# Kernel optimization log

Measured on AMD Instinct MI355X. Metric: run time of the kernel, lower is better.

The kernel has to match this reference:

```python
import jax, jax.numpy as jnp
import numpy as np

N, D, K = 131072, 128, 256
MAX_ITER = 8
TOL = 1e-4


def setup_inputs() -> dict:
    key = jax.random.key(0)
    kx, kp = jax.random.split(key)
    X = jax.random.normal(kx, (N, D), dtype=jnp.float32)
    # torch.randperm(N)[:K] -> distinct initial centroid indices
    init_idx = jax.random.permutation(kp, N)[:K]
    return {"X": X, "init_idx": init_idx, "max_iter": MAX_ITER}


def _assign(X, centroids):
    # argmin over Euclidean distance == argmin over squared distance;
    # ||x||^2 is constant per row so drop it: d2[n,k] = ||c_k||^2 - 2 x_n . c_k
    d2 = jnp.sum(centroids * centroids, axis=1)[None, :] - 2.0 * (X @ centroids.T)  # [N,K]
    return jnp.argmin(d2, axis=1)  # [N]


def reference(X, init_idx, max_iter):
    n = X.shape[0]
    centroids0 = X[init_idx]  # [K,D]

    def step(carry, _):
        centroids, done = carry
        labels = _assign(X, centroids)  # [N]
        sums = jax.ops.segment_sum(X, labels, num_segments=K)  # [K,D]
        counts = jax.ops.segment_sum(jnp.ones((n,), X.dtype), labels, num_segments=K)  # [K]
        new_c = sums / counts[:, None]  # empty cluster -> 0/0 = nan (matches torch mean of empty)
        shift = jnp.linalg.norm(new_c - centroids)
        new_done = jnp.logical_or(done, shift < TOL)
        # torch breaks BEFORE assigning new centroids when converged
        centroids = jnp.where(new_done, centroids, new_c)
        return (centroids, new_done), labels

    (centroids, _), labels_hist = jax.lax.scan(
        step, (centroids0, jnp.array(False)), None, length=max_iter
    )
    labels = labels_hist[-1]
    return labels, centroids
```

## Files before the change

kernel.cpp:

```cpp
#include <hip/hip_runtime.h>

#define NP 131072
#define DD 128
#define KK 256
#define MAXIT 8
#define TOLSQ (1e-4f * 1e-4f)
#define POSB 256
#define UPIPE 8

typedef _Float16 half8 __attribute__((ext_vector_type(8)));
typedef float f32x4 __attribute__((ext_vector_type(4)));

__device__ __forceinline__ void async_copy16(const void* g, void* l) {
    __builtin_amdgcn_global_load_lds(
        (const __attribute__((address_space(1))) void*)g,
        (__attribute__((address_space(3))) void*)l, 16, 0, 0);
}

struct Ws {
    float C[KK * DD];
    float newC[KK * DD];
    float cnorm[KK];
    float sums[KK * DD];
    float shiftsq;
    int done;
    int ilab[NP];
    int counts[KK];
    int cursor[KK];
    int ordlab[NP];
    alignas(16) _Float16 Csh[KK * DD];
    alignas(16) _Float16 Csl[KK * DD];
    alignas(16) _Float16 Xsh[(size_t)NP * DD];
    alignas(16) _Float16 Xsl[(size_t)NP * DD];
};

__global__ void k_init(const float* __restrict__ X, const int* __restrict__ idx,
                       float* __restrict__ C, int* __restrict__ done) {
    int k = blockIdx.x, d = threadIdx.x;
    C[k * DD + d] = X[(size_t)idx[k] * DD + d];
    if (k == 0 && d == 0) *done = 0;
}

__global__ void k_split(const float* __restrict__ X, _Float16* __restrict__ Xh,
                        _Float16* __restrict__ Xl) {
    size_t idx = (size_t)blockIdx.x * 256 + threadIdx.x;
    int lane = idx & 63;
    size_t g16k = idx >> 6;
    size_t point = (g16k >> 2) * 16 + (lane & 15);
    int dim0 = (int)(g16k & 3) * 32 + (lane >> 4) * 8;
    const f32x4* s4 = (const f32x4*)(X + point * DD + dim0);
    f32x4 a = s4[0], b = s4[1];
    half8 h, l;
#pragma unroll
    for (int j = 0; j < 4; j++) {
        _Float16 hi = (_Float16)a[j];
        h[j] = hi; l[j] = (_Float16)(a[j] - (float)hi);
    }
#pragma unroll
    for (int j = 0; j < 4; j++) {
        _Float16 hi = (_Float16)b[j];
        h[4 + j] = hi; l[4 + j] = (_Float16)(b[j] - (float)hi);
    }
    *(half8*)(Xh + idx * 8) = h;
    *(half8*)(Xl + idx * 8) = l;
}

__global__ void k_prep0(const float* __restrict__ C, float* __restrict__ cnorm,
                        _Float16* __restrict__ Ch, _Float16* __restrict__ Cl,
                        int* __restrict__ counts, int* __restrict__ cursor) {
    int k = blockIdx.x, d = threadIdx.x;
    float v = C[k * DD + d];
    _Float16 hi = (_Float16)v;
    int ct = k >> 4, l4 = k & 15, ks = d >> 5, q = (d >> 3) & 3, j = d & 7;
    size_t dst = ((size_t)(ks * 16 + ct) * 64 + (q * 16 + l4)) * 8 + j;
    Ch[dst] = hi;
    Cl[dst] = (_Float16)(v - (float)hi);
    __shared__ float red[DD];
    red[d] = v * v;
    __syncthreads();
    for (int s = DD / 2; s > 0; s >>= 1) {
        if (d < s) red[d] += red[d + s];
        __syncthreads();
    }
    if (d == 0) {
        cnorm[k] = red[0];
        counts[k] = 0;
        cursor[k] = 0;
    }
}

__global__ __launch_bounds__(256, 2) void k_assign(
    const _Float16* __restrict__ Xh, const _Float16* __restrict__ Xl,
    const _Float16* __restrict__ Ch, const _Float16* __restrict__ Cl,
    const float* __restrict__ cnorm, float* __restrict__ outlab,
    int* __restrict__ ilab, int* __restrict__ counts,
    float* __restrict__ shiftsq) {
    __shared__ __align__(16) _Float16 Bls[2 * 2 * 16 * 64 * 8];
    __shared__ int hist[KK];
    if (blockIdx.x == 0 && threadIdx.x == 0) *shiftsq = 0.0f;
    hist[threadIdx.x] = 0;

    const int wave = threadIdx.x >> 6;
    const int lane = threadIdx.x & 63;
    const int l4 = lane & 15, g = lane >> 4;
    const int g16 = blockIdx.x * 8 + wave * 2;
    char* const lds = (char*)Bls;

    auto stage = [&](int ks, int buf) {
        char* dst = lds + buf * 32768;
#pragma unroll
        for (int j = 0; j < 4; j++) {
            const int slot = j * 256 + wave * 64;
            async_copy16(Ch + (size_t)ks * 8192 + (size_t)(slot + lane) * 8,
                         dst + (size_t)slot * 16);
            async_copy16(Cl + (size_t)ks * 8192 + (size_t)(slot + lane) * 8,
                         dst + 16384 + (size_t)slot * 16);
        }
    };

    f32x4 acc[2][16];
#pragma unroll
    for (int pg = 0; pg < 2; pg++)
#pragma unroll
        for (int ct = 0; ct < 16; ct++) acc[pg][ct] = (f32x4){0.f, 0.f, 0.f, 0.f};

    stage(0, 0);
    __syncthreads();

#pragma unroll 1
    for (int ks = 0; ks < 4; ks++) {
        if (ks < 3) stage(ks + 1, (ks + 1) & 1);

        const size_t a0 = ((size_t)(g16 * 4 + ks) * 64 + lane) * 8;
        const size_t a1 = ((size_t)((g16 + 1) * 4 + ks) * 64 + lane) * 8;
        half8 ah0 = *(const half8*)(Xh + a0);
        half8 al0 = *(const half8*)(Xl + a0);
        half8 ah1 = *(const half8*)(Xh + a1);
        half8 al1 = *(const half8*)(Xl + a1);

        char* cur = lds + (ks & 1) * 32768;
#pragma unroll
        for (int ct = 0; ct < 16; ct++) {
            half8 bh = *(const half8*)(cur + ct * 1024 + lane * 16);
            half8 bl = *(const half8*)(cur + 16384 + ct * 1024 + lane * 16);
            acc[0][ct] = __builtin_amdgcn_mfma_f32_16x16x32_f16(al0, bh, acc[0][ct], 0, 0, 0);
            acc[0][ct] = __builtin_amdgcn_mfma_f32_16x16x32_f16(ah0, bl, acc[0][ct], 0, 0, 0);
            acc[0][ct] = __builtin_amdgcn_mfma_f32_16x16x32_f16(ah0, bh, acc[0][ct], 0, 0, 0);
            acc[1][ct] = __builtin_amdgcn_mfma_f32_16x16x32_f16(al1, bh, acc[1][ct], 0, 0, 0);
            acc[1][ct] = __builtin_amdgcn_mfma_f32_16x16x32_f16(ah1, bl, acc[1][ct], 0, 0, 0);
            acc[1][ct] = __builtin_amdgcn_mfma_f32_16x16x32_f16(ah1, bh, acc[1][ct], 0, 0, 0);
        }
        __syncthreads();
    }

    float cn[16];
#pragma unroll
    for (int ct = 0; ct < 16; ct++) cn[ct] = cnorm[ct * 16 + l4];

    unsigned long long best[2][4];
#pragma unroll
    for (int pg = 0; pg < 2; pg++)
#pragma unroll
        for (int r = 0; r < 4; r++) best[pg][r] = ~0ull;

#pragma unroll
    for (int pg = 0; pg < 2; pg++)
#pragma unroll
        for (int ct = 0; ct < 16; ct++)
#pragma unroll
            for (int r = 0; r < 4; r++) {
                float s = fmaf(-2.0f, acc[pg][ct][r], cn[ct]);
                if (__builtin_isnan(s)) s = -__builtin_inff();
                unsigned u = __float_as_uint(s);
                unsigned m = (u >> 31) ? ~u : (u ^ 0x80000000u);
                unsigned long long key =
                    ((unsigned long long)m << 32) | (unsigned)(ct * 16 + l4);
                if (key < best[pg][r]) best[pg][r] = key;
            }

#pragma unroll
    for (int d = 1; d < 16; d <<= 1)
#pragma unroll
        for (int pg = 0; pg < 2; pg++)
#pragma unroll
            for (int r = 0; r < 4; r++) {
                unsigned long long o = __shfl_xor(best[pg][r], d, 64);
                if (o < best[pg][r]) best[pg][r] = o;
            }

    __syncthreads();
    if (l4 == 0) {
#pragma unroll
        for (int pg = 0; pg < 2; pg++)
#pragma unroll
            for (int r = 0; r < 4; r++) {
                int point = blockIdx.x * 128 + wave * 32 + pg * 16 + g * 4 + r;
                int lbl = (int)(best[pg][r] & 0x1ff);
                outlab[point] = (float)lbl;
                ilab[point] = lbl;
                atomicAdd(&hist[lbl], 1);
            }
    }
    __syncthreads();
    int h = hist[threadIdx.x];
    if (h) atomicAdd(&counts[threadIdx.x], h);
}

__global__ __launch_bounds__(256) void k_scatter(
    const int* __restrict__ ilab, const int* __restrict__ counts,
    int* __restrict__ cursor, int* __restrict__ ordlab,
    float* __restrict__ sums) {
    const int t = threadIdx.x;
    const int b = blockIdx.x;

    if (t < 128) sums[b * 128 + t] = 0.0f;

    __shared__ int hist[KK];
    __shared__ int pre[KK];
    __shared__ int gbase[KK];
    hist[t] = 0;
    int c = counts[t];
    pre[t] = c;
    __syncthreads();

    const int p0 = b * 512;
    const int la = ilab[p0 + t];
    const int lb = ilab[p0 + 256 + t];
    atomicAdd(&hist[la], 1);
    atomicAdd(&hist[lb], 1);

#pragma unroll
    for (int d = 1; d < KK; d <<= 1) {
        int v = (t >= d) ? pre[t - d] : 0;
        __syncthreads();
        pre[t] += v;
        __syncthreads();
    }
    int h = hist[t];
    int gb = (pre[t] - c) + (h ? atomicAdd(&cursor[t], h) : 0);
    gbase[t] = gb;
    __syncthreads();
    hist[t] = 0;
    __syncthreads();

    int ra = atomicAdd(&hist[la], 1);
    ordlab[gbase[la] + ra] = (p0 + t) | (la << 17);
    int rb = atomicAdd(&hist[lb], 1);
    ordlab[gbase[lb] + rb] = (p0 + 256 + t) | (lb << 17);
}

__global__ __launch_bounds__(256) void k_sum(
    const float* __restrict__ X, const int* __restrict__ ordlab,
    float* __restrict__ sums) {
    const int t = threadIdx.x;
    const int d = t & 127, h = t >> 7;

    __shared__ int sol[POSB];
    sol[t] = ordlab[blockIdx.x * POSB + t];
    __syncthreads();

    const int PP = POSB / 2;
    float xv[UPIPE], xn[UPIPE];
#pragma unroll
    for (int u = 0; u < UPIPE; u++)
        xv[u] = X[(size_t)(sol[2 * u + h] & 0x1ffff) * DD + d];

    float acc = 0.0f;
    int cur = sol[h] >> 17;

    for (int jb = 0; jb < PP; jb += UPIPE) {
#pragma unroll
        for (int u = 0; u < UPIPE; u++) {
            int nj = jb + u + UPIPE;
            int o = sol[2 * (nj < PP ? nj : PP - 1) + h];
            xn[u] = X[(size_t)(o & 0x1ffff) * DD + d];
        }
#pragma unroll
        for (int u = 0; u < UPIPE; u++) {
            int l = sol[2 * (jb + u) + h] >> 17;
            if (l != cur) {
                atomicAdd(&sums[cur * DD + d], acc);
                acc = 0.0f;
                cur = l;
            }
            acc += xv[u];
        }
#pragma unroll
        for (int u = 0; u < UPIPE; u++) xv[u] = xn[u];
    }
    atomicAdd(&sums[cur * DD + d], acc);
}

__global__ void k_reduce(const float* __restrict__ sums, const int* __restrict__ counts,
                         const float* __restrict__ C, float* __restrict__ newC,
                         float* __restrict__ shiftsq) {
    const int g = blockIdx.x * 256 + threadIdx.x;
    const int k = g >> 7;
    const int t = threadIdx.x;

    float nc = sums[g] / (float)counts[k];
    newC[g] = nc;
    float diff = nc - C[g];

    __shared__ float red[256];
    red[t] = diff * diff;
    __syncthreads();
    for (int st = 128; st > 0; st >>= 1) {
        if (t < st) red[t] += red[t + st];
        __syncthreads();
    }
    if (t == 0) atomicAdd(shiftsq, red[0]);
}

__global__ void k_upprep(const float* __restrict__ newC, float* __restrict__ C,
                         const float* __restrict__ shiftsq, int* __restrict__ done,
                         float* __restrict__ cnorm, _Float16* __restrict__ Ch,
                         _Float16* __restrict__ Cl, int* __restrict__ counts,
                         int* __restrict__ cursor) {
    const int t = threadIdx.x;
    const int k = blockIdx.x * 2 + (t >> 7);
    const int d = t & 127;
    float ss = *shiftsq;
    int nd = (*done != 0) || (ss < TOLSQ);
    float v = nd ? C[k * DD + d] : newC[k * DD + d];
    C[k * DD + d] = v;
    if (blockIdx.x == 0 && t == 0 && nd) *done = 1;
    if (d == 0) {
        counts[k] = 0;
        cursor[k] = 0;
    }

    _Float16 hi = (_Float16)v;
    int ct = k >> 4, l4 = k & 15, ks = d >> 5, q = (d >> 3) & 3, j = d & 7;
    size_t dst = ((size_t)(ks * 16 + ct) * 64 + (q * 16 + l4)) * 8 + j;
    Ch[dst] = hi;
    Cl[dst] = (_Float16)(v - (float)hi);

    __shared__ float red[256];
    red[t] = v * v;
    __syncthreads();
    for (int s = 64; s > 0; s >>= 1) {
        if ((t & 127) < s) red[t] += red[t + s];
        __syncthreads();
    }
    if (d == 0) cnorm[k] = red[t];
}

__global__ void k_final(const float* __restrict__ C, float* __restrict__ out) {
    int i = blockIdx.x * 256 + threadIdx.x;
    out[i] = C[i];
}

extern "C" void kernel_launch(void* const* d_in, const int* in_sizes, int n_in,
                              void* d_out, int out_size, void* d_ws, size_t ws_size,
                              hipStream_t stream) {
    const float* X = (const float*)d_in[0];
    const int* idx = (const int*)d_in[1];
    float* out = (float*)d_out;
    Ws* w = (Ws*)d_ws;

    k_init<<<KK, DD, 0, stream>>>(X, idx, w->C, &w->done);
    k_split<<<(int)((size_t)NP * DD / 8 / 256), 256, 0, stream>>>(X, w->Xsh, w->Xsl);
    k_prep0<<<KK, DD, 0, stream>>>(w->C, w->cnorm, w->Csh, w->Csl, w->counts, w->cursor);

    for (int it = 0; it < MAXIT; it++) {
        k_assign<<<NP / 128, 256, 0, stream>>>(w->Xsh, w->Xsl, w->Csh, w->Csl,
                                               w->cnorm, out, w->ilab, w->counts,
                                               &w->shiftsq);
        k_scatter<<<NP / 512, 256, 0, stream>>>(w->ilab, w->counts, w->cursor,
                                                w->ordlab, w->sums);
        k_sum<<<NP / POSB, 256, 0, stream>>>(X, w->ordlab, w->sums);
        k_reduce<<<KK * DD / 256, 256, 0, stream>>>(w->sums, w->counts, w->C,
                                                    w->newC, &w->shiftsq);
        k_upprep<<<KK / 2, 256, 0, stream>>>(w->newC, w->C, &w->shiftsq, &w->done,
                                             w->cnorm, w->Csh, w->Csl, w->counts,
                                             w->cursor);
    }

    k_final<<<KK * DD / 256, 256, 0, stream>>>(w->C, out + NP);
}
```

Measured before the change: 723.5 us.

## Load all centroids into LDS once per block and loop over point tiles

The assign kernel now runs 512-thread blocks that copy the full split-fp16 centroid matrix (128 KB) into LDS once, then each wave processes two point tiles. This replaces per-k-slice double-buffered staging and the syncthreads between slices, and register-prefetches the next X slice. It amortises centroid loads over four times more points per block and removes barriers. The cost is a 128 KB LDS footprint, which may limit occupancy to one block per CU despite the launch bounds requesting two.

```diff
diff --git a/kernel.cpp b/kernel.cpp
--- a/kernel.cpp
+++ b/kernel.cpp
@@ -89,121 +89,132 @@
     }
 }
 
-__global__ __launch_bounds__(256, 2) void k_assign(
+__global__ __launch_bounds__(512, 2) void k_assign(
     const _Float16* __restrict__ Xh, const _Float16* __restrict__ Xl,
     const _Float16* __restrict__ Ch, const _Float16* __restrict__ Cl,
     const float* __restrict__ cnorm, float* __restrict__ outlab,
     int* __restrict__ ilab, int* __restrict__ counts,
     float* __restrict__ shiftsq) {
-    __shared__ __align__(16) _Float16 Bls[2 * 2 * 16 * 64 * 8];
+    __shared__ __align__(16) _Float16 B[2 * KK * DD];
     __shared__ int hist[KK];
-    if (blockIdx.x == 0 && threadIdx.x == 0) *shiftsq = 0.0f;
-    hist[threadIdx.x] = 0;
-
-    const int wave = threadIdx.x >> 6;
-    const int lane = threadIdx.x & 63;
+    const int tid = threadIdx.x;
+    const int wave = tid >> 6;
+    const int lane = tid & 63;
     const int l4 = lane & 15, g = lane >> 4;
-    const int g16 = blockIdx.x * 8 + wave * 2;
-    char* const lds = (char*)Bls;
-
-    auto stage = [&](int ks, int buf) {
-        char* dst = lds + buf * 32768;
-#pragma unroll
-        for (int j = 0; j < 4; j++) {
-            const int slot = j * 256 + wave * 64;
-            async_copy16(Ch + (size_t)ks * 8192 + (size_t)(slot + lane) * 8,
-                         dst + (size_t)slot * 16);
-            async_copy16(Cl + (size_t)ks * 8192 + (size_t)(slot + lane) * 8,
-                         dst + 16384 + (size_t)slot * 16);
-        }
-    };
-
-    f32x4 acc[2][16];
-#pragma unroll
-    for (int pg = 0; pg < 2; pg++)
-#pragma unroll
-        for (int ct = 0; ct < 16; ct++) acc[pg][ct] = (f32x4){0.f, 0.f, 0.f, 0.f};
-
-    stage(0, 0);
+
+    if (blockIdx.x == 0 && tid == 0) *shiftsq = 0.0f;
+    if (tid < KK) hist[tid] = 0;
+
+    char* const lds = (char*)B;
+#pragma unroll
+    for (int r = 0; r < 8; r++) {
+        const int slot = r * 512 + wave * 64;
+        async_copy16(Ch + (size_t)(slot + lane) * 8, lds + (size_t)slot * 16);
+        async_copy16(Cl + (size_t)(slot + lane) * 8,
+                     lds + 65536 + (size_t)slot * 16);
+    }
+
+    float cn[16];
+#pragma unroll
+    for (int ct = 0; ct < 16; ct++) cn[ct] = cnorm[ct * 16 + l4];
+
     __syncthreads();
 
 #pragma unroll 1
-    for (int ks = 0; ks < 4; ks++) {
-        if (ks < 3) stage(ks + 1, (ks + 1) & 1);
-
-        const size_t a0 = ((size_t)(g16 * 4 + ks) * 64 + lane) * 8;
-        const size_t a1 = ((size_t)((g16 + 1) * 4 + ks) * 64 + lane) * 8;
+    for (int t = 0; t < 2; t++) {
+        const int g16 = blockIdx.x * 32 + t * 16 + wave * 2;
+
+        f32x4 acc[2][16];
+#pragma unroll
+        for (int pg = 0; pg < 2; pg++)
+#pragma unroll
+            for (int ct = 0; ct < 16; ct++) acc[pg][ct] = (f32x4){0.f, 0.f, 0.f, 0.f};
+
+        size_t a0 = ((size_t)(g16 * 4 + 0) * 64 + lane) * 8;
+        size_t a1 = ((size_t)((g16 + 1) * 4 + 0) * 64 + lane) * 8;
         half8 ah0 = *(const half8*)(Xh + a0);
         half8 al0 = *(const half8*)(Xl + a0);
         half8 ah1 = *(const half8*)(Xh + a1);
         half8 al1 = *(const half8*)(Xl + a1);
 
-        char* cur = lds + (ks & 1) * 32768;
-#pragma unroll
-        for (int ct = 0; ct < 16; ct++) {
-            half8 bh = *(const half8*)(cur + ct * 1024 + lane * 16);
-            half8 bl = *(const half8*)(cur + 16384 + ct * 1024 + lane * 16);
-            acc[0][ct] = __builtin_amdgcn_mfma_f32_16x16x32_f16(al0, bh, acc[0][ct], 0, 0, 0);
-            acc[0][ct] = __builtin_amdgcn_mfma_f32_16x16x32_f16(ah0, bl, acc[0][ct], 0, 0, 0);
-            acc[0][ct] = __builtin_amdgcn_mfma_f32_16x16x32_f16(ah0, bh, acc[0][ct], 0, 0, 0);
-            acc[1][ct] = __builtin_amdgcn_mfma_f32_16x16x32_f16(al1, bh, acc[1][ct], 0, 0, 0);
-            acc[1][ct] = __builtin_amdgcn_mfma_f32_16x16x32_f16(ah1, bl, acc[1][ct], 0, 0, 0);
-            acc[1][ct] = __builtin_amdgcn_mfma_f32_16x16x32_f16(ah1, bh, acc[1][ct], 0, 0, 0);
+#pragma unroll 1
+        for (int ks = 0; ks < 4; ks++) {
+            half8 nh0, nl0, nh1, nl1;
+            if (ks < 3) {
+                const size_t b0 = ((size_t)(g16 * 4 + ks + 1) * 64 + lane) * 8;
+                const size_t b1 = ((size_t)((g16 + 1) * 4 + ks + 1) * 64 + lane) * 8;
+                nh0 = *(const half8*)(Xh + b0);
+                nl0 = *(const half8*)(Xl + b0);
+                nh1 = *(const half8*)(Xh + b1);
+                nl1 = *(const half8*)(Xl + b1);
+            }
+
+            char* const curh = lds + ks * 16384;
+            char* const curl = lds + 65536 + ks * 16384;
+#pragma unroll
+            for (int ct = 0; ct < 16; ct++) {
+                half8 bh = *(const half8*)(curh + ct * 1024 + lane * 16);
+                half8 bl = *(const half8*)(curl + ct * 1024 + lane * 16);
+                acc[0][ct] = __builtin_amdgcn_mfma_f32_16x16x32_f16(al0, bh, acc[0][ct], 0, 0, 0);
+                acc[0][ct] = __builtin_amdgcn_mfma_f32_16x16x32_f16(ah0, bl, acc[0][ct], 0, 0, 0);
+                acc[0][ct] = __builtin_amdgcn_mfma_f32_16x16x32_f16(ah0, bh, acc[0][ct], 0, 0, 0);
+                acc[1][ct] = __builtin_amdgcn_mfma_f32_16x16x32_f16(al1, bh, acc[1][ct], 0, 0, 0);
+                acc[1][ct] = __builtin_amdgcn_mfma_f32_16x16x32_f16(ah1, bl, acc[1][ct], 0, 0, 0);
+                acc[1][ct] = __builtin_amdgcn_mfma_f32_16x16x32_f16(ah1, bh, acc[1][ct], 0, 0, 0);
+            }
+            ah0 = nh0; al0 = nl0; ah1 = nh1; al1 = nl1;
         }
-        __syncthreads();
-    }
-
-    float cn[16];
-#pragma unroll
-    for (int ct = 0; ct < 16; ct++) cn[ct] = cnorm[ct * 16 + l4];
-
-    unsigned long long best[2][4];
-#pragma unroll
-    for (int pg = 0; pg < 2; pg++)
-#pragma unroll
-        for (int r = 0; r < 4; r++) best[pg][r] = ~0ull;
-
-#pragma unroll
-    for (int pg = 0; pg < 2; pg++)
-#pragma unroll
-        for (int ct = 0; ct < 16; ct++)
-#pragma unroll
-            for (int r = 0; r < 4; r++) {
-                float s = fmaf(-2.0f, acc[pg][ct][r], cn[ct]);
-                if (__builtin_isnan(s)) s = -__builtin_inff();
-                unsigned u = __float_as_uint(s);
-                unsigned m = (u >> 31) ? ~u : (u ^ 0x80000000u);
-                unsigned long long key =
-                    ((unsigned long long)m << 32) | (unsigned)(ct * 16 + l4);
-                if (key < best[pg][r]) best[pg][r] = key;
-            }
-
-#pragma unroll
-    for (int d = 1; d < 16; d <<= 1)
+
+        unsigned long long best[2][4];
 #pragma unroll
         for (int pg = 0; pg < 2; pg++)
 #pragma unroll
-            for (int r = 0; r < 4; r++) {
-                unsigned long long o = __shfl_xor(best[pg][r], d, 64);
-                if (o < best[pg][r]) best[pg][r] = o;
-            }
-
-    __syncthreads();
-    if (l4 == 0) {
+            for (int r = 0; r < 4; r++) best[pg][r] = ~0ull;
+
 #pragma unroll
         for (int pg = 0; pg < 2; pg++)
 #pragma unroll
-            for (int r = 0; r < 4; r++) {
-                int point = blockIdx.x * 128 + wave * 32 + pg * 16 + g * 4 + r;
-                int lbl = (int)(best[pg][r] & 0x1ff);
-                outlab[point] = (float)lbl;
-                ilab[point] = lbl;
-                atomicAdd(&hist[lbl], 1);
-            }
-    }
-    __syncthreads();
-    int h = hist[threadIdx.x];
-    if (h) atomicAdd(&counts[threadIdx.x], h);
+            for (int ct = 0; ct < 16; ct++)
+#pragma unroll
+                for (int r = 0; r < 4; r++) {
+                    float s = fmaf(-2.0f, acc[pg][ct][r], cn[ct]);
+                    if (__builtin_isnan(s)) s = -__builtin_inff();
+                    unsigned u = __float_as_uint(s);
+                    unsigned m = (u >> 31) ? ~u : (u ^ 0x80000000u);
+                    unsigned long long key =
+                        ((unsigned long long)m << 32) | (unsigned)(ct * 16 + l4);
+                    if (key < best[pg][r]) best[pg][r] = key;
+                }
+
+#pragma unroll
+        for (int d = 1; d < 16; d <<= 1)
+#pragma unroll
+            for (int pg = 0; pg < 2; pg++)
+#pragma unroll
+                for (int r = 0; r < 4; r++) {
+                    unsigned long long o = __shfl_xor(best[pg][r], d, 64);
+                    if (o < best[pg][r]) best[pg][r] = o;
+                }
+
+        if (l4 == 0) {
+#pragma unroll
+            for (int pg = 0; pg < 2; pg++)
+#pragma unroll
+                for (int r = 0; r < 4; r++) {
+                    int point = (g16 + pg) * 16 + g * 4 + r;
+                    int lbl = (int)(best[pg][r] & 0x1ff);
+                    outlab[point] = (float)lbl;
+                    ilab[point] = lbl;
+                    atomicAdd(&hist[lbl], 1);
+                }
+        }
+    }
+
+    __syncthreads();
+    if (tid < KK) {
+        int h = hist[tid];
+        if (h) atomicAdd(&counts[tid], h);
+    }
 }
 
 __global__ __launch_bounds__(256) void k_scatter(
@@ -364,7 +375,7 @@
     k_prep0<<<KK, DD, 0, stream>>>(w->C, w->cnorm, w->Csh, w->Csl, w->counts, w->cursor);
 
     for (int it = 0; it < MAXIT; it++) {
-        k_assign<<<NP / 128, 256, 0, stream>>>(w->Xsh, w->Xsl, w->Csh, w->Csl,
+        k_assign<<<NP / 512, 512, 0, stream>>>(w->Xsh, w->Xsl, w->Csh, w->Csl,
                                                w->cnorm, out, w->ilab, w->counts,
                                                &w->shiftsq);
         k_scatter<<<NP / 512, 256, 0, stream>>>(w->ilab, w->counts, w->cursor,
```

Result: faster. 653.8 us (-9.6%).
